# Kernel tuning notes

Measured on AMD Instinct MI355X. Metric: run time of the kernel, lower is better.

Reference implementation:

```python
import jax, jax.numpy as jnp
import numpy as np

DIM = 1024          # n_embd
NUM_EXPERTS = 8
TOP_K = 2
HIDDEN = 4 * DIM // TOP_K   # expert_hidden_dim = 2048
BS, SLEN = 1, 2048


def setup_inputs() -> dict:
    key = jax.random.key(0)
    k0, k1, k2, k3 = jax.random.split(key, 4)
    x = jax.random.normal(k0, (BS, SLEN, DIM), dtype=jnp.float32)
    gate_w = jax.random.normal(k1, (NUM_EXPERTS, DIM), dtype=jnp.float32) * 0.02
    w_up = jax.random.normal(k2, (NUM_EXPERTS, HIDDEN, DIM), dtype=jnp.float32) * 0.02
    w_down = jax.random.normal(k3, (NUM_EXPERTS, DIM, HIDDEN), dtype=jnp.float32) * 0.02
    expert_bias = jnp.zeros((NUM_EXPERTS,), dtype=jnp.float32)
    return {"x": x, "gate_w": gate_w, "w_up": w_up, "w_down": w_down,
            "expert_bias": expert_bias}


def _moe(x, gate_w, w_up, w_down, expert_bias):
    bs, slen, dim = x.shape
    xf = x.reshape(-1, dim)                       # (T, D)
    # Sigmoid router (scores in fp32, bias only affects selection, not weights)
    scores = jax.nn.sigmoid(xf @ gate_w.T)        # (T, E)
    biased = scores + expert_bias
    _, sel = jax.lax.top_k(biased, TOP_K)         # (T, K) expert ids, distinct per token
    top_scores = jnp.take_along_axis(scores, sel, axis=-1)  # (T, K)

    # Scatter/gather dispatch + grouped GEMM is mathematically equivalent to:
    #   out[t] = sum_k W_down[e_tk] @ relu(W_up[e_tk] @ (s_tk * x[t]))^2
    # Loop over the small fixed expert set via lax.scan; unassigned tokens
    # contribute exactly zero (relu(0)^2 = 0), honoring the routing sparsity.
    def body(acc, ew):
        e, wu, wd = ew
        # combined routing weight for this expert per token (at most one slot)
        w_t = jnp.sum(jnp.where(sel == e, top_scores, 0.0), axis=-1)  # (T,)
        xe = xf * w_t[:, None]                    # (T, D), zero for non-routed
        h = jnp.square(jax.nn.relu(xe @ wu.T))    # (T, H)  relu(x)^2 activation
        return acc + h @ wd.T, None

    out0 = jnp.zeros_like(xf)
    out, _ = jax.lax.scan(body, out0, (jnp.arange(NUM_EXPERTS), w_up, w_down))
    return out.reshape(bs, slen, dim)


def reference(x, gate_w, w_up, w_down, expert_bias):
    return _moe(x, gate_w, w_up, w_down, expert_bias)
```

## Files before the change

kernel.cpp:

```cpp
#include <hip/hip_runtime.h>
#include <cstdint>
#include <cstddef>

#define T_TOK 2048
#define DMODEL 1024
#define NEXP 8
#define HID 2048
#define DUMP_ID 4096

typedef __bf16 bf16x8 __attribute__((ext_vector_type(8)));
typedef float f32x4 __attribute__((ext_vector_type(4)));
typedef unsigned short u16;
typedef u16 u16x8 __attribute__((ext_vector_type(8)));

__device__ __forceinline__ u16 f2bf(float f) {
    union { float f; unsigned int u; } v; v.f = f;
    unsigned int u = v.u;
    unsigned int r = (u + 0x7FFFu + ((u >> 16) & 1u)) >> 16;
    return (u16)r;
}

__device__ __forceinline__ void gl2lds16(const void* g, void* l) {
    __builtin_amdgcn_global_load_lds(
        (const __attribute__((address_space(1))) void*)g,
        (__attribute__((address_space(3))) void*)l,
        16, 0, 0);
}

__global__ __launch_bounds__(256) void fused_pre(
    const float4* __restrict__ x4, const float4* __restrict__ gw4,
    const float* __restrict__ bias, ushort4* __restrict__ xb4,
    unsigned int* __restrict__ selpack, float* __restrict__ w2,
    unsigned int* __restrict__ xb_dump_row_u32) {
    const int b = blockIdx.x;
    const int tid = threadIdx.x;

    if (b == 256) {
        if (tid < DMODEL / 2) xb_dump_row_u32[tid] = 0;
        return;
    }
    const int wv = tid >> 6;
    const int lane = tid & 63;
    const int pair = b * 4 + wv;
    const int t0 = 2 * pair, t1 = t0 + 1;

    float acc0[NEXP], acc1[NEXP];
#pragma unroll
    for (int e = 0; e < NEXP; ++e) { acc0[e] = 0.f; acc1[e] = 0.f; }
#pragma unroll
    for (int j = 0; j < 4; ++j) {
        int i4 = lane + j * 64;
        float4 a0 = x4[t0 * 256 + i4];
        float4 a1 = x4[t1 * 256 + i4];
        ushort4 s0, s1;
        s0.x = f2bf(a0.x); s0.y = f2bf(a0.y); s0.z = f2bf(a0.z); s0.w = f2bf(a0.w);
        s1.x = f2bf(a1.x); s1.y = f2bf(a1.y); s1.z = f2bf(a1.z); s1.w = f2bf(a1.w);
        xb4[t0 * 256 + i4] = s0;
        xb4[t1 * 256 + i4] = s1;
#pragma unroll
        for (int e = 0; e < NEXP; ++e) {
            float4 g = gw4[e * 256 + i4];
            acc0[e] += a0.x * g.x + a0.y * g.y + a0.z * g.z + a0.w * g.w;
            acc1[e] += a1.x * g.x + a1.y * g.y + a1.z * g.z + a1.w * g.w;
        }
    }
#pragma unroll
    for (int e = 0; e < NEXP; ++e)
        for (int off = 32; off > 0; off >>= 1) {
            acc0[e] += __shfl_xor(acc0[e], off, 64);
            acc1[e] += __shfl_xor(acc1[e], off, 64);
        }
    if (lane == 0) {
#pragma unroll
        for (int tt = 0; tt < 2; ++tt) {
            int t = tt ? t1 : t0;
            float sc[NEXP], bi[NEXP];
#pragma unroll
            for (int e = 0; e < NEXP; ++e) {
                float a = tt ? acc1[e] : acc0[e];
                sc[e] = 1.f / (1.f + expf(-a));
                bi[e] = sc[e] + bias[e];
            }
            int e0 = 0;
            for (int e = 1; e < NEXP; ++e) if (bi[e] > bi[e0]) e0 = e;
            int e1 = -1;
            for (int e = 0; e < NEXP; ++e) {
                if (e == e0) continue;
                if (e1 < 0 || bi[e] > bi[e1]) e1 = e;
            }
            selpack[t] = (unsigned int)e0 | ((unsigned int)e1 << 8);
            w2[2 * t]     = sc[e0] * sc[e0];
            w2[2 * t + 1] = sc[e1] * sc[e1];
        }
    }
}

__global__ __launch_bounds__(256) void build_lists(
    const unsigned int* __restrict__ selpack, int* __restrict__ counts,
    int* __restrict__ list) {
    const int e = blockIdx.x;
    const int tid = threadIdx.x;
    const int lane = tid & 63;
    const int wv = tid >> 6;
    __shared__ int wsum[4];
    __shared__ int base;
    if (tid == 0) base = 0;
    __syncthreads();
    for (int tb = 0; tb < T_TOK; tb += 256) {
        int t = tb + tid;
        unsigned int sp = selpack[t];
        bool f1 = ((sp >> 8) & 255u) == (unsigned)e;
        bool f = ((sp & 255u) == (unsigned)e) | f1;
        int id = 2 * t + (f1 ? 1 : 0);
        unsigned long long m = __ballot(f);
        int pos = __popcll(m & ((1ull << lane) - 1ull));
        if (lane == 0) wsum[wv] = __popcll(m);
        __syncthreads();
        int woff = 0;
#pragma unroll
        for (int i = 0; i < 4; ++i) if (i < wv) woff += wsum[i];
        int bse = base;
        if (f) list[e * T_TOK + bse + woff + pos] = id;
        __syncthreads();
        if (tid == 0) base = bse + wsum[0] + wsum[1] + wsum[2] + wsum[3];
    }
    __syncthreads();
    int total = base;
    if (tid == 0) counts[e] = total;
    for (int i = total + tid; i < T_TOK; i += 256) list[e * T_TOK + i] = DUMP_ID;
}

template <int MODE>
__global__ __launch_bounds__(256, 2) void moe_gemm(
    const u16* __restrict__ Asrc, const int* __restrict__ list,
    const int* __restrict__ counts, const float* __restrict__ Ball32,
    const float* __restrict__ w2, u16* __restrict__ Hout,
    float* __restrict__ Cout) {
    constexpr int K   = (MODE == 0) ? DMODEL : HID;
    constexpr int N   = (MODE == 0) ? HID : DMODEL;
    constexpr int NKT = K / 64;
    constexpr int NTN = N / 128;
    constexpr int LOGNTN = (MODE == 0) ? 4 : 3;

    const int b = blockIdx.x;
    const int e = b & 7;
    const int rest = b >> 3;
    const int m0 = (rest >> LOGNTN) * 128;
    if (m0 >= counts[e]) return;
    const int n0 = (rest & (NTN - 1)) * 128;

    const int tid = threadIdx.x;
    const int lane = tid & 63;
    const int w = tid >> 6;

    __shared__ u16 As[128 * 64];
    __shared__ u16 Bs[128 * 64];

    const int* mylist = list + e * T_TOK + m0;
    const float* B32 = Ball32 + (size_t)e * HID * DMODEL;

    const u16* ap[4];
    const float4* bp[4];
    int bwr[4];
    const int c8 = tid & 7;
#pragma unroll
    for (int it = 0; it < 4; ++it) {
        int row = it * 32 + (tid >> 3);
        int gs = c8 ^ (row & 7);
        int id = mylist[row];
        int arow = (MODE == 0) ? (id >> 1) : id;
        ap[it] = Asrc + (size_t)arow * K + gs * 8;
        bp[it] = (const float4*)(B32 + (size_t)(n0 + row) * K) + c8 * 2;
        bwr[it] = row * 64 + gs * 8;
    }

    const int wm = (w >> 1) * 64;
    const int wn = (w & 1) * 64;
    const int quad = lane >> 4;
    const int lrow = lane & 15;

    f32x4 acc[4][4];
#pragma unroll
    for (int i = 0; i < 4; ++i)
#pragma unroll
        for (int j = 0; j < 4; ++j) acc[i][j] = f32x4{0.f, 0.f, 0.f, 0.f};

    for (int kt = 0; kt < NKT; ++kt) {
#pragma unroll
        for (int it = 0; it < 4; ++it)
            gl2lds16(ap[it] + kt * 64, &As[(it * 256 + w * 64) * 8]);
        float4 bu[4][2];
#pragma unroll
        for (int it = 0; it < 4; ++it) {
            bu[it][0] = bp[it][kt * 16];
            bu[it][1] = bp[it][kt * 16 + 1];
        }
#pragma unroll
        for (int it = 0; it < 4; ++it) {
            u16x8 o;
            o[0] = f2bf(bu[it][0].x); o[1] = f2bf(bu[it][0].y);
            o[2] = f2bf(bu[it][0].z); o[3] = f2bf(bu[it][0].w);
            o[4] = f2bf(bu[it][1].x); o[5] = f2bf(bu[it][1].y);
            o[6] = f2bf(bu[it][1].z); o[7] = f2bf(bu[it][1].w);
            *(u16x8*)&Bs[bwr[it]] = o;
        }
        __syncthreads();
#pragma unroll
        for (int s = 0; s < 2; ++s) {
            const int q = s * 4 + quad;
            bf16x8 af[4], bfr[4];
#pragma unroll
            for (int i = 0; i < 4; ++i) {
                int ra = wm + i * 16 + lrow;
                int rb = wn + i * 16 + lrow;
                af[i]  = *(const bf16x8*)&As[ra * 64 + (q ^ (ra & 7)) * 8];
                bfr[i] = *(const bf16x8*)&Bs[rb * 64 + (q ^ (rb & 7)) * 8];
            }
#pragma unroll
            for (int i = 0; i < 4; ++i)
#pragma unroll
                for (int j = 0; j < 4; ++j)
                    acc[i][j] = __builtin_amdgcn_mfma_f32_16x16x32_bf16(
                        af[i], bfr[j], acc[i][j], 0, 0, 0);
        }
        __syncthreads();
    }

#pragma unroll
    for (int i = 0; i < 4; ++i) {
        int mbase = wm + i * 16 + (lane >> 4) * 4;
        int ids[4];
        float ww[4];
#pragma unroll
        for (int r = 0; r < 4; ++r) {
            ids[r] = mylist[mbase + r];
            if (MODE == 0) ww[r] = w2[ids[r]];
        }
#pragma unroll
        for (int j = 0; j < 4; ++j) {
            int n = n0 + wn + j * 16 + (lane & 15);
#pragma unroll
            for (int r = 0; r < 4; ++r) {
                float v = acc[i][j][r];
                if (MODE == 0) {
                    v = (v > 0.f) ? v * v * ww[r] : 0.f;
                    Hout[(size_t)ids[r] * HID + n] = f2bf(v);
                } else {
                    if (ids[r] != DUMP_ID)
                        atomicAdd(&Cout[(size_t)(ids[r] >> 1) * DMODEL + n], v);
                }
            }
        }
    }
}

extern "C" void kernel_launch(void* const* d_in, const int* in_sizes, int n_in,
                              void* d_out, int out_size, void* d_ws, size_t ws_size,
                              hipStream_t stream) {
    const float* x      = (const float*)d_in[0];
    const float* gate_w = (const float*)d_in[1];
    const float* w_up   = (const float*)d_in[2];
    const float* w_down = (const float*)d_in[3];
    const float* bias   = (const float*)d_in[4];
    float* out = (float*)d_out;

    char* p = (char*)d_ws;
    int* counts = (int*)p;                 p += 256;
    int* list   = (int*)p;                 p += NEXP * T_TOK * 4;
    float* w2   = (float*)p;               p += 4104 * 4;
    unsigned int* selpack = (unsigned int*)p;  p += T_TOK * 4;
    u16* xb  = (u16*)p;  p += (size_t)(T_TOK + 1) * DMODEL * 2;
    u16* h   = (u16*)p;  p += (size_t)(2 * T_TOK + 1) * HID * 2;

    hipMemsetAsync(d_out, 0, (size_t)out_size * sizeof(float), stream);

    fused_pre<<<257, 256, 0, stream>>>(
        (const float4*)x, (const float4*)gate_w, bias,
        (ushort4*)xb, selpack, w2,
        (unsigned int*)(xb + (size_t)T_TOK * DMODEL));

    build_lists<<<NEXP, 256, 0, stream>>>(selpack, counts, list);

    moe_gemm<0><<<16 * (HID / 128) * NEXP, 256, 0, stream>>>(
        xb, list, counts, w_up, w2, h, nullptr);

    moe_gemm<1><<<16 * (DMODEL / 128) * NEXP, 256, 0, stream>>>(
        h, list, counts, w_down, w2, nullptr, out);
}
```

Baseline: 258.6 us.

## Double-buffer LDS tiles in MoE GEMM and split-K the down projection

Adds double-buffered shared-memory tiles so the global loads for the next K tile (async A to LDS, B into registers) are issued before computing the current tile, overlapping memory latency with MFMA work. Also splits the K dimension of the down-projection GEMM in two, doubling its grid so more blocks fill the GPU. Split-K relies on the epilogue accumulating into the zeroed output atomically. Doubled LDS use may lower occupancy under launch_bounds(256,2).

```diff
diff --git a/kernel.cpp b/kernel.cpp
--- a/kernel.cpp
+++ b/kernel.cpp
@@ -141,20 +141,25 @@
     constexpr int NKT = K / 64;
     constexpr int NTN = N / 128;
     constexpr int LOGNTN = (MODE == 0) ? 4 : 3;
+    constexpr int KSP = (MODE == 0) ? 1 : 2;
+    constexpr int KTPER = NKT / KSP;
 
     const int b = blockIdx.x;
     const int e = b & 7;
     const int rest = b >> 3;
-    const int m0 = (rest >> LOGNTN) * 128;
+    const int n0 = (rest & (NTN - 1)) * 128;
+    const int rest2 = rest >> LOGNTN;
+    const int m0 = (rest2 & 15) * 128;
+    const int ks = rest2 >> 4;
     if (m0 >= counts[e]) return;
-    const int n0 = (rest & (NTN - 1)) * 128;
+    const int kt0 = ks * KTPER, kt1 = kt0 + KTPER;
 
     const int tid = threadIdx.x;
     const int lane = tid & 63;
     const int w = tid >> 6;
 
-    __shared__ u16 As[128 * 64];
-    __shared__ u16 Bs[128 * 64];
+    __shared__ u16 As[2][128 * 64];
+    __shared__ u16 Bs[2][128 * 64];
 
     const int* mylist = list + e * T_TOK + m0;
     const float* B32 = Ball32 + (size_t)e * HID * DMODEL;
@@ -185,16 +190,21 @@
 #pragma unroll
         for (int j = 0; j < 4; ++j) acc[i][j] = f32x4{0.f, 0.f, 0.f, 0.f};
 
-    for (int kt = 0; kt < NKT; ++kt) {
+    float4 bu[4][2];
+
+    auto stageA = [&](int kt, int buf) {
 #pragma unroll
         for (int it = 0; it < 4; ++it)
-            gl2lds16(ap[it] + kt * 64, &As[(it * 256 + w * 64) * 8]);
-        float4 bu[4][2];
+            gl2lds16(ap[it] + kt * 64, &As[buf][(it * 256 + w * 64) * 8]);
+    };
+    auto loadB = [&](int kt) {
 #pragma unroll
         for (int it = 0; it < 4; ++it) {
             bu[it][0] = bp[it][kt * 16];
             bu[it][1] = bp[it][kt * 16 + 1];
         }
+    };
+    auto writeB = [&](int buf) {
 #pragma unroll
         for (int it = 0; it < 4; ++it) {
             u16x8 o;
@@ -202,9 +212,10 @@
             o[2] = f2bf(bu[it][0].z); o[3] = f2bf(bu[it][0].w);
             o[4] = f2bf(bu[it][1].x); o[5] = f2bf(bu[it][1].y);
             o[6] = f2bf(bu[it][1].z); o[7] = f2bf(bu[it][1].w);
-            *(u16x8*)&Bs[bwr[it]] = o;
-        }
-        __syncthreads();
+            *(u16x8*)&Bs[buf][bwr[it]] = o;
+        }
+    };
+    auto compute = [&](int buf) {
 #pragma unroll
         for (int s = 0; s < 2; ++s) {
             const int q = s * 4 + quad;
@@ -213,8 +224,8 @@
             for (int i = 0; i < 4; ++i) {
                 int ra = wm + i * 16 + lrow;
                 int rb = wn + i * 16 + lrow;
-                af[i]  = *(const bf16x8*)&As[ra * 64 + (q ^ (ra & 7)) * 8];
-                bfr[i] = *(const bf16x8*)&Bs[rb * 64 + (q ^ (rb & 7)) * 8];
+                af[i]  = *(const bf16x8*)&As[buf][ra * 64 + (q ^ (ra & 7)) * 8];
+                bfr[i] = *(const bf16x8*)&Bs[buf][rb * 64 + (q ^ (rb & 7)) * 8];
             }
 #pragma unroll
             for (int i = 0; i < 4; ++i)
@@ -223,6 +234,23 @@
                     acc[i][j] = __builtin_amdgcn_mfma_f32_16x16x32_bf16(
                         af[i], bfr[j], acc[i][j], 0, 0, 0);
         }
+    };
+
+    stageA(kt0, 0);
+    loadB(kt0);
+    writeB(0);
+    __syncthreads();
+
+    for (int kt = kt0; kt < kt1; ++kt) {
+        const int cur = (kt - kt0) & 1;
+        const int nxt = cur ^ 1;
+        const bool more = (kt + 1 < kt1);
+        if (more) {
+            stageA(kt + 1, nxt);
+            loadB(kt + 1);
+        }
+        compute(cur);
+        if (more) writeB(nxt);
         __syncthreads();
     }
 
@@ -284,6 +312,6 @@
     moe_gemm<0><<<16 * (HID / 128) * NEXP, 256, 0, stream>>>(
         xb, list, counts, w_up, w2, h, nullptr);
 
-    moe_gemm<1><<<16 * (DMODEL / 128) * NEXP, 256, 0, stream>>>(
+    moe_gemm<1><<<2 * 16 * (DMODEL / 128) * NEXP, 256, 0, stream>>>(
         h, list, counts, w_down, w2, nullptr, out);
 }
```

Measured after the change: 271.2 us. 4.9% more time.

## Replace down-proj atomics with per-slot partials and a combine kernel

Applied to the files above, without the earlier changes.

The down-projection GEMM no longer atomically accumulates into the output. Each routed slot now writes its result to its own fp32 partial row, and a new combine kernel sums the two slots per token, which also removes the output memset. The hidden activations are stored in a compact per-expert row layout, so the second GEMM reads its A rows contiguously instead of gathering them through the token list. The cost is a larger workspace, an extra kernel launch, and an extra full read/write pass over the partial buffer.

```diff
diff --git a/kernel.cpp b/kernel.cpp
--- a/kernel.cpp
+++ b/kernel.cpp
@@ -135,11 +135,10 @@
     const u16* __restrict__ Asrc, const int* __restrict__ list,
     const int* __restrict__ counts, const float* __restrict__ Ball32,
     const float* __restrict__ w2, u16* __restrict__ Hout,
-    float* __restrict__ Cout) {
+    float* __restrict__ Pout) {
     constexpr int K   = (MODE == 0) ? DMODEL : HID;
-    constexpr int N   = (MODE == 0) ? HID : DMODEL;
     constexpr int NKT = K / 64;
-    constexpr int NTN = N / 128;
+    constexpr int NTN = ((MODE == 0) ? HID : DMODEL) / 128;
     constexpr int LOGNTN = (MODE == 0) ? 4 : 3;
 
     const int b = blockIdx.x;
@@ -167,9 +166,12 @@
     for (int it = 0; it < 4; ++it) {
         int row = it * 32 + (tid >> 3);
         int gs = c8 ^ (row & 7);
-        int id = mylist[row];
-        int arow = (MODE == 0) ? (id >> 1) : id;
-        ap[it] = Asrc + (size_t)arow * K + gs * 8;
+        if (MODE == 0) {
+            int id = mylist[row];
+            ap[it] = Asrc + (size_t)(id >> 1) * K + gs * 8;
+        } else {
+            ap[it] = Asrc + (size_t)(e * T_TOK + m0 + row) * K + gs * 8;
+        }
         bp[it] = (const float4*)(B32 + (size_t)(n0 + row) * K) + c8 * 2;
         bwr[it] = row * 64 + gs * 8;
     }
@@ -244,14 +246,27 @@
                 float v = acc[i][j][r];
                 if (MODE == 0) {
                     v = (v > 0.f) ? v * v * ww[r] : 0.f;
-                    Hout[(size_t)ids[r] * HID + n] = f2bf(v);
+                    Hout[(size_t)(e * T_TOK + m0 + mbase + r) * HID + n] = f2bf(v);
                 } else {
                     if (ids[r] != DUMP_ID)
-                        atomicAdd(&Cout[(size_t)(ids[r] >> 1) * DMODEL + n], v);
+                        Pout[(size_t)ids[r] * DMODEL + n] = v;
                 }
             }
         }
     }
+}
+
+__global__ __launch_bounds__(256) void combine(
+    const float4* __restrict__ part4, float4* __restrict__ out4) {
+    int idx = blockIdx.x * 256 + threadIdx.x;
+    int t = idx >> 8;
+    int d4 = idx & 255;
+    float4 p0 = part4[(size_t)(2 * t) * 256 + d4];
+    float4 p1 = part4[(size_t)(2 * t + 1) * 256 + d4];
+    float4 o;
+    o.x = p0.x + p1.x; o.y = p0.y + p1.y;
+    o.z = p0.z + p1.z; o.w = p0.w + p1.w;
+    out4[idx] = o;
 }
 
 extern "C" void kernel_launch(void* const* d_in, const int* in_sizes, int n_in,
@@ -270,9 +285,8 @@
     float* w2   = (float*)p;               p += 4104 * 4;
     unsigned int* selpack = (unsigned int*)p;  p += T_TOK * 4;
     u16* xb  = (u16*)p;  p += (size_t)(T_TOK + 1) * DMODEL * 2;
-    u16* h   = (u16*)p;  p += (size_t)(2 * T_TOK + 1) * HID * 2;
-
-    hipMemsetAsync(d_out, 0, (size_t)out_size * sizeof(float), stream);
+    u16* h   = (u16*)p;  p += (size_t)NEXP * T_TOK * HID * 2;
+    float* part = (float*)p;  p += (size_t)2 * T_TOK * DMODEL * 4;
 
     fused_pre<<<257, 256, 0, stream>>>(
         (const float4*)x, (const float4*)gate_w, bias,
@@ -285,5 +299,8 @@
         xb, list, counts, w_up, w2, h, nullptr);
 
     moe_gemm<1><<<16 * (DMODEL / 128) * NEXP, 256, 0, stream>>>(
-        h, list, counts, w_down, w2, nullptr, out);
-}
+        h, list, counts, w_down, w2, nullptr, part);
+
+    combine<<<T_TOK * DMODEL / 4 / 256, 256, 0, stream>>>(
+        (const float4*)part, (float4*)out);
+}
```

New measurement: 255.0 us. Within noise of the previous version (-1.4%).
